# Performance work log

Hardware: AMD Instinct MI355X
Metric: run time of the kernel (lower is better)

The kernel has to match this reference:

```python
import jax, jax.numpy as jnp
import numpy as np

BN_EPS = 1e-5

def conv2d(x, w, pad):
    return jax.lax.conv_general_dilated(x, w, (1, 1), [(pad, pad), (pad, pad)],
                                        dimension_numbers=('NCHW', 'OIHW', 'NCHW'))

def bn(x, g, b, m, v):
    # eval-mode batchnorm with running stats
    c = (None, slice(None), None, None)
    return g[c] * (x - m[c]) * jax.lax.rsqrt(v[c] + BN_EPS) + b[c]

def criss_cross_attention(x, wq, wk, wv, gamma):
    # x: (B, C, H, W); q/k have reduced dim d = C//8
    B, C, H, W = x.shape
    q = jnp.einsum('bchw,dc->bdhw', x, wq)
    k = jnp.einsum('bchw,dc->bdhw', x, wk)
    v = jnp.einsum('bchw,dc->bdhw', x, wv)
    # column (vertical) affinities: for each (h,w), keys at (k,w) -> (B,H,W,H)
    eH = jnp.einsum('bdhw,bdkw->bhwk', q, k)
    # -inf on the h==k diagonal (avoid counting the center pixel twice)
    eH = eH + jnp.where(jnp.eye(H, dtype=bool), -jnp.inf, 0.0)[None, :, None, :]
    # row (horizontal) affinities: keys at (h,k) -> (B,H,W,W)
    eW = jnp.einsum('bdhw,bdhk->bhwk', q, k)
    att = jax.nn.softmax(jnp.concatenate([eH, eW], axis=3), axis=3)  # (B,H,W,H+W)
    aH, aW = att[..., :H], att[..., H:]
    oH = jnp.einsum('bhwk,bdkw->bdhw', aH, v)
    oW = jnp.einsum('bhwk,bdhk->bdhw', aW, v)
    return gamma * (oH + oW) + x

def upsample_bilinear_align_corners(x, out_h, out_w):
    # torch nn.Upsample(mode='bilinear', align_corners=True)
    def interp(x, size, axis):
        n = x.shape[axis]
        pos = jnp.arange(size, dtype=x.dtype) * ((n - 1) / (size - 1))
        lo = jnp.floor(pos).astype(jnp.int32)
        hi = jnp.minimum(lo + 1, n - 1)
        w = pos - lo.astype(x.dtype)
        shp = [1] * x.ndim; shp[axis] = size
        w = w.reshape(shp)
        return jnp.take(x, lo, axis=axis) * (1 - w) + jnp.take(x, hi, axis=axis) * w
    x = interp(x, out_h, 2)
    return interp(x, out_w, 3)

def setup_inputs() -> dict:
    key = jax.random.key(0)
    ks = jax.random.split(key, 16)
    B, C, H, W = 2, 2048, 96, 96
    ic = C // 32          # inter_c = 64
    dq = ic // 8          # 8
    nc = 19
    s = 0.05
    return {
        'x': jax.random.normal(ks[0], (B, C, H, W), jnp.float32),
        'w_in': jax.random.normal(ks[1], (ic, C, 3, 3), jnp.float32) * s,
        'bn_in_g': jnp.ones((ic,), jnp.float32),
        'bn_in_b': jnp.zeros((ic,), jnp.float32),
        'bn_in_m': jax.random.normal(ks[2], (ic,), jnp.float32) * 0.1,
        'bn_in_v': jax.random.uniform(ks[3], (ic,), jnp.float32, 0.5, 1.5),
        'wq': jax.random.normal(ks[4], (dq, ic), jnp.float32) * s,
        'wk': jax.random.normal(ks[5], (dq, ic), jnp.float32) * s,
        'wv': jax.random.normal(ks[6], (ic, ic), jnp.float32) * s,
        'cca_gamma': jax.random.uniform(ks[7], (1,), jnp.float32, 0.2, 0.8),
        'w_out': jax.random.normal(ks[8], (ic, ic, 3, 3), jnp.float32) * s,
        'bn_out_g': jnp.ones((ic,), jnp.float32),
        'bn_out_b': jnp.zeros((ic,), jnp.float32),
        'bn_out_m': jax.random.normal(ks[9], (ic,), jnp.float32) * 0.1,
        'bn_out_v': jax.random.uniform(ks[10], (ic,), jnp.float32, 0.5, 1.5),
        'w_cls1': jax.random.normal(ks[11], (ic, C + ic, 3, 3), jnp.float32) * s,
        'bn_cls_g': jnp.ones((ic,), jnp.float32),
        'bn_cls_b': jnp.zeros((ic,), jnp.float32),
        'bn_cls_m': jax.random.normal(ks[12], (ic,), jnp.float32) * 0.1,
        'bn_cls_v': jax.random.uniform(ks[13], (ic,), jnp.float32, 0.5, 1.5),
        'w_cls2': jax.random.normal(ks[14], (nc, ic, 1, 1), jnp.float32) * s,
    }

def reference(x, w_in, bn_in_g, bn_in_b, bn_in_m, bn_in_v,
              wq, wk, wv, cca_gamma,
              w_out, bn_out_g, bn_out_b, bn_out_m, bn_out_v,
              w_cls1, bn_cls_g, bn_cls_b, bn_cls_m, bn_cls_v, w_cls2):
    RECURRENCE = 2
    out = jax.nn.relu(bn(conv2d(x, w_in, 1), bn_in_g, bn_in_b, bn_in_m, bn_in_v))
    for _ in range(RECURRENCE):
        out = criss_cross_attention(out, wq, wk, wv, cca_gamma)
    out = jax.nn.relu(bn(conv2d(out, w_out, 1), bn_out_g, bn_out_b, bn_out_m, bn_out_v))
    out = jnp.concatenate([x, out], axis=1)
    # cls_seg: conv -> BN (no relu) -> upsample x8 (bilinear, align_corners) -> 1x1 conv
    out = bn(conv2d(out, w_cls1, 1), bn_cls_g, bn_cls_b, bn_cls_m, bn_cls_v)
    H, W = out.shape[2], out.shape[3]
    out = upsample_bilinear_align_corners(out, H * 8, W * 8)
    out = conv2d(out, w_cls2, 0)
    return out
```

## Files before the change

kernel.cpp:

```cpp
#include <hip/hip_runtime.h>
#include <stdint.h>

#define HW 9216

typedef float f32x4 __attribute__((ext_vector_type(4)));
typedef short s16x8 __attribute__((ext_vector_type(8)));

#define PIN() asm volatile("" ::: "memory")
#define WAITV12() asm volatile("s_waitcnt vmcnt(12)" ::: "memory")

__device__ __forceinline__ unsigned short f2bf(float f){
  union { float fv; uint32_t u; } x; x.fv = f;
  uint32_t u = x.u;
  u += 0x7fffu + ((u >> 16) & 1u);
  return (unsigned short)(u >> 16);
}
__device__ __forceinline__ float bf2f(unsigned short s){
  union { uint32_t u; float fv; } x; x.u = ((uint32_t)s) << 16;
  return x.fv;
}

__device__ __forceinline__ void gload16(const void* g, void* l){
  __builtin_amdgcn_global_load_lds(
    (const __attribute__((address_space(1))) unsigned int*)g,
    (__attribute__((address_space(3))) unsigned int*)l, 16, 0, 0);
}

__global__ __launch_bounds__(256) void transp_kernel(const float* __restrict__ x,
    unsigned short* __restrict__ xT){
  __shared__ unsigned short tl[256 * 66];
  int blk = blockIdx.x;
  int b = blk / 1152; int r = blk - b * 1152;
  int cchunk = r / 144, pxt = r - cchunk * 144;
  int c0 = cchunk * 256, px0 = pxt * 64;
  int tid = threadIdx.x;
  for (int e = tid; e < 4096; e += 256){
    int cc = e >> 4, pq = e & 15;
    float4 v4 = *(const float4*)(x + ((size_t)(b * 2048 + c0 + cc)) * HW + px0 + pq * 4);
    const float* vp = (const float*)&v4;
    #pragma unroll
    for (int j = 0; j < 4; j++) tl[cc * 66 + pq * 4 + j] = f2bf(vp[j]);
  }
  __syncthreads();
  for (int j = tid; j < 2048; j += 256){
    int px = j >> 5, oct = j & 31;
    s16x8 pk;
    #pragma unroll
    for (int t = 0; t < 8; t++) pk[t] = (short)tl[(oct * 8 + t) * 66 + px];
    *(s16x8*)(xT + ((size_t)(b * 9216 + px0 + px)) * 2048 + c0 + oct * 8) = pk;
  }
}

__global__ void pack_all_kernel(const float* __restrict__ w_in, const float* __restrict__ w_out,
    const float* __restrict__ w_cls1, unsigned short* __restrict__ WpIn,
    unsigned short* __restrict__ WpOut, unsigned short* __restrict__ WpCls){
  const int N0 = 64 * 2048 * 9, N1 = 64 * 64 * 9, N2 = 64 * 2112 * 9;
  int total = N0 + N1 + N2;
  for (int i = blockIdx.x * blockDim.x + threadIdx.x; i < total; i += gridDim.x * blockDim.x){
    const float* w; unsigned short* Wp; int Cin; int idx;
    if (i < N0){ w = w_in; Wp = WpIn; Cin = 2048; idx = i; }
    else if (i < N0 + N1){ w = w_out; Wp = WpOut; Cin = 64; idx = i - N0; }
    else { w = w_cls1; Wp = WpCls; Cin = 2112; idx = i - N0 - N1; }
    int c = idx & 31; int r = idx >> 5; int o = r & 63; int r2 = r >> 6;
    int tap = r2 % 9; int ck = r2 / 9;
    Wp[idx] = f2bf(w[((size_t)o * Cin + ck * 32 + c) * 9 + tap]);
  }
}

template<int T>
__device__ __forceinline__ void tapbody(const char* hb, s16x8 (&bs)[4], f32x4 (&acc)[4][4],
    const unsigned short* wbase, int gmax, int g0, int wv, int ln, int kg){
  constexpr int dy = T / 3, dx = T - dy * 3;
  #pragma unroll
  for (int mf = 0; mf < 4; mf++){
    int p = (wv * 4 + mf + dy) * 18 + (ln + dx);
    int aoff = p * 64 + ((kg ^ (p & 3)) << 4);
    s16x8 a = *(const s16x8*)(hb + aoff);
    #pragma unroll
    for (int nf = 0; nf < 4; nf++)
      acc[mf][nf] = __builtin_amdgcn_mfma_f32_16x16x32_bf16(a, bs[nf], acc[mf][nf], 0, 0, 0);
  }
  constexpr int dck = (T + 3) / 9, dt = (T + 3) % 9;
  if (g0 + T + 3 < gmax){
    const unsigned short* wb2 = wbase + dck * 18432 + dt * 2048;
    #pragma unroll
    for (int nf = 0; nf < 4; nf++) bs[nf] = *(const s16x8*)(wb2 + nf * 512);
  }
}

__global__ __launch_bounds__(256, 2) void conv_nhwc_kernel(
    const unsigned short* __restrict__ A0, int c0stride,
    const unsigned short* __restrict__ A1, int nck0,
    const unsigned short* __restrict__ Wp,
    unsigned short* __restrict__ sl, int nchunks,
    const unsigned short* __restrict__ zp){
  int mt = blockIdx.x;
  int b = mt / 36; int r = mt - b * 36;
  int h0 = (r / 6) * 16, w0 = (r % 6) * 16;
  int KS = gridDim.y, ks = blockIdx.y;
  int c0 = (nchunks * ks) / KS, c1 = (nchunks * (ks + 1)) / KS;
  int tid = threadIdx.x, lane = tid & 63, wv = tid >> 6;
  int ln = lane & 15, kg = lane >> 4;
  __shared__ char halo[2][24576];

  int pixb0[6], pixb1[6]; bool val[6];
  #pragma unroll
  for (int rr = 0; rr < 6; rr++){
    int i = tid + rr * 256;
    int p = i >> 2, q_lds = i & 3;
    int logq = q_lds ^ (p & 3);
    int hh = p / 18, ww = p - hh * 18;
    int h = h0 - 1 + hh, w = w0 - 1 + ww;
    bool v = (i < 1296) && ((unsigned)h < 96u) && ((unsigned)w < 96u);
    val[rr] = v;
    int pix = (b * 96 + h) * 96 + w;
    pixb0[rr] = v ? (pix * c0stride * 2 + logq * 16) : 0;
    pixb1[rr] = v ? (pix * 128 + logq * 16) : 0;
  }
  const char* a0B = (const char*)A0;
  const char* a1B = (const char*)A1;
  const char* zpB = (const char*)zp;

  auto stage = [&](char* ldsB, int ck){
    bool inA0 = (ck < nck0);
    int chb0 = ck * 64, chb1 = (ck - nck0) * 64;
    #pragma unroll
    for (int rr = 0; rr < 6; rr++){
      const char* src = zpB;
      if (val[rr]) src = inA0 ? (a0B + pixb0[rr] + chb0) : (a1B + pixb1[rr] + chb1);
      gload16(src, ldsB + (tid + rr * 256) * 16);
    }
  };

  f32x4 acc[4][4];
  #pragma unroll
  for (int i = 0; i < 4; i++)
    #pragma unroll
    for (int j = 0; j < 4; j++) acc[i][j] = (f32x4)(0.f);

  s16x8 bs0[4], bs1[4], bs2[4];
  int gmax = (c1 - c0) * 9;

  stage(&halo[0][0], c0);
  PIN();
  {
    const unsigned short* w0b = Wp + (size_t)c0 * 18432 + ln * 32 + kg * 8;
    #pragma unroll
    for (int nf = 0; nf < 4; nf++){
      bs0[nf] = *(const s16x8*)(w0b + 0 * 2048 + nf * 512);
      bs1[nf] = *(const s16x8*)(w0b + 1 * 2048 + nf * 512);
      bs2[nf] = *(const s16x8*)(w0b + 2 * 2048 + nf * 512);
    }
  }
  WAITV12();
  __builtin_amdgcn_s_barrier();

  for (int ck = c0; ck < c1; ck++){
    int cur = (ck - c0) & 1;
    if (ck + 1 < c1){ stage(&halo[cur ^ 1][0], ck + 1); PIN(); }
    const unsigned short* wbase = Wp + (size_t)ck * 18432 + ln * 32 + kg * 8;
    const char* hb = &halo[cur][0];
    int g0 = (ck - c0) * 9;
    tapbody<0>(hb, bs0, acc, wbase, gmax, g0, wv, ln, kg);
    tapbody<1>(hb, bs1, acc, wbase, gmax, g0, wv, ln, kg);
    tapbody<2>(hb, bs2, acc, wbase, gmax, g0, wv, ln, kg);
    tapbody<3>(hb, bs0, acc, wbase, gmax, g0, wv, ln, kg);
    tapbody<4>(hb, bs1, acc, wbase, gmax, g0, wv, ln, kg);
    tapbody<5>(hb, bs2, acc, wbase, gmax, g0, wv, ln, kg);
    tapbody<6>(hb, bs0, acc, wbase, gmax, g0, wv, ln, kg);
    tapbody<7>(hb, bs1, acc, wbase, gmax, g0, wv, ln, kg);
    tapbody<8>(hb, bs2, acc, wbase, gmax, g0, wv, ln, kg);
    if (ck + 1 < c1){
      WAITV12();
      __builtin_amdgcn_s_barrier();
    }
  }

  unsigned short* base = sl + ((size_t)(ks * 72 + mt)) * 16384;
  #pragma unroll
  for (int mf = 0; mf < 4; mf++)
    #pragma unroll
    for (int nf = 0; nf < 4; nf++){
      int o = nf * 16 + ln;
      #pragma unroll
      for (int rr = 0; rr < 4; rr++){
        int m = wv * 64 + mf * 16 + kg * 4 + rr;
        base[m * 64 + o] = f2bf(acc[mf][nf][rr]);
      }
    }
}

__global__ __launch_bounds__(256) void bn_reduce_kernel(const unsigned short* __restrict__ sl,
    int KS, const float* __restrict__ g, const float* __restrict__ bb,
    const float* __restrict__ mm, const float* __restrict__ vv, int relu,
    unsigned short* __restrict__ out, int do_proj,
    const float* __restrict__ wq, const float* __restrict__ wk, const float* __restrict__ wv,
    float* __restrict__ q, float* __restrict__ k, unsigned short* __restrict__ v){
  __shared__ float yl[4 * 65];
  __shared__ float wqL[8 * 65], wkL[8 * 65], wvL[64 * 65];
  int tid = threadIdx.x;
  if (do_proj){
    for (int i = tid; i < 512; i += 256){
      int d = i >> 6, c = i & 63;
      wqL[d * 65 + c] = wq[i]; wkL[d * 65 + c] = wk[i];
    }
    for (int i = tid; i < 4096; i += 256){
      int o = i >> 6, c = i & 63;
      wvL[o * 65 + c] = wv[i];
    }
  }
  int idx = blockIdx.x * 256 + tid;
  int mt = idx >> 14, e = idx & 16383;
  int m = e >> 6, o = e & 63;
  float s = 0.f;
  for (int ks = 0; ks < KS; ks++) s += bf2f(sl[((size_t)(ks * 72 + mt)) * 16384 + e]);
  float sc = g[o] * rsqrtf(vv[o] + 1e-5f);
  float valf = (s - mm[o]) * sc + bb[o];
  if (relu) valf = fmaxf(valf, 0.f);
  int b = mt / 36; int r = mt - b * 36;
  int h = (r / 6) * 16 + (m >> 4), w = (r % 6) * 16 + (m & 15);
  out[(((size_t)b * 96 + h) * 96 + w) * 64 + o] = f2bf(valf);
  if (do_proj){
    int px = tid >> 6;
    yl[px * 65 + o] = valf;
    __syncthreads();
    int m2 = ((blockIdx.x & 63) << 2) + px;
    int h2 = (r / 6) * 16 + (m2 >> 4), w2 = (r % 6) * 16 + (m2 & 15);
    size_t pix2 = ((size_t)b * 96 + h2) * 96 + w2;
    float va = 0.f;
    #pragma unroll 8
    for (int c = 0; c < 64; c++) va += wvL[o * 65 + c] * yl[px * 65 + c];
    v[pix2 * 64 + o] = f2bf(va);
    if (o < 16){
      const float* wsel = (o < 8) ? wqL : wkL;
      int d = o & 7;
      float qa = 0.f;
      #pragma unroll 8
      for (int c = 0; c < 64; c++) qa += wsel[d * 65 + c] * yl[px * 65 + c];
      if (o < 8) q[pix2 * 8 + d] = qa; else k[pix2 * 8 + d] = qa;
    }
  }
}

__global__ __launch_bounds__(256) void bn_reduce_cls_kernel(const unsigned short* __restrict__ sl,
    int KS, const float* __restrict__ g, const float* __restrict__ bb,
    const float* __restrict__ mm, const float* __restrict__ vv,
    const float* __restrict__ w2, float* __restrict__ t19){
  __shared__ float yl[4][64];
  __shared__ float w2L[19 * 64];
  int tid = threadIdx.x;
  for (int i = tid; i < 1216; i += 256) w2L[i] = w2[i];
  int idx = blockIdx.x * 256 + tid;
  int mt = idx >> 14, e = idx & 16383;
  int o = e & 63;
  float s = 0.f;
  for (int ks = 0; ks < KS; ks++) s += bf2f(sl[((size_t)(ks * 72 + mt)) * 16384 + e]);
  float sc = g[o] * rsqrtf(vv[o] + 1e-5f);
  float valf = (s - mm[o]) * sc + bb[o];
  yl[tid >> 6][o] = valf;
  __syncthreads();
  if (tid < 76){
    int mq = tid / 19, j = tid - mq * 19;
    float a = 0.f;
    #pragma unroll 8
    for (int c = 0; c < 64; c++) a += w2L[j * 64 + c] * yl[mq][c];
    int m = ((blockIdx.x & 63) << 2) + mq;
    int b = mt / 36; int r = mt - b * 36;
    int h = (r / 6) * 16 + (m >> 4), w = (r % 6) * 16 + (m & 15);
    t19[((size_t)(b * 19 + j)) * HW + h * 96 + w] = a;
  }
}

__global__ __launch_bounds__(256) void cca_proj_kernel(const unsigned short* __restrict__ xin,
    const float* __restrict__ wq, const float* __restrict__ wk, const float* __restrict__ wv,
    float* __restrict__ q, float* __restrict__ k, unsigned short* __restrict__ v){
  __shared__ float wqL[512], wkL[512], wvL[4096];
  int tid = threadIdx.x;
  for (int i = tid; i < 512; i += 256){ wqL[i] = wq[i]; wkL[i] = wk[i]; }
  for (int i = tid; i < 4096; i += 256) wvL[i] = wv[i];
  __syncthreads();
  int gid = blockIdx.x * 256 + tid;
  int gp = gid >> 1, half = gid & 1;
  unsigned short xv16[64];
  #pragma unroll
  for (int t = 0; t < 8; t++)
    *(s16x8*)(&xv16[t * 8]) = *(const s16x8*)(xin + (size_t)gp * 64 + t * 8);
  float qa[4], ka[4], va[32];
  #pragma unroll
  for (int d = 0; d < 4; d++){ qa[d] = 0.f; ka[d] = 0.f; }
  #pragma unroll
  for (int d = 0; d < 32; d++) va[d] = 0.f;
  int qo = half * 4, vo = half * 32;
  #pragma unroll 4
  for (int c = 0; c < 64; c++){
    float xv = bf2f(xv16[c]);
    #pragma unroll
    for (int d = 0; d < 4; d++){ qa[d] += wqL[(qo + d) * 64 + c] * xv; ka[d] += wkL[(qo + d) * 64 + c] * xv; }
    #pragma unroll
    for (int d = 0; d < 32; d++) va[d] += wvL[(vo + d) * 64 + c] * xv;
  }
  #pragma unroll
  for (int d = 0; d < 4; d++){ q[(size_t)gp * 8 + qo + d] = qa[d]; k[(size_t)gp * 8 + qo + d] = ka[d]; }
  #pragma unroll
  for (int t = 0; t < 4; t++){
    s16x8 pk;
    #pragma unroll
    for (int j = 0; j < 8; j++) pk[j] = (short)f2bf(va[t * 8 + j]);
    *(s16x8*)(v + (size_t)gp * 64 + vo + t * 8) = pk;
  }
}

__global__ __launch_bounds__(256, 2) void cca_colE_kernel(const float* __restrict__ qT,
    const float* __restrict__ kT, float* __restrict__ ebuf){
  int blk = blockIdx.x;
  int b = blk / 192; int r = blk - b * 192; int w = r >> 1, z = r & 1;
  __shared__ float qcL[96 * 12], kcL[48 * 12];
  int tid = threadIdx.x;
  for (int i = tid; i < 768; i += 256){
    int hp = i >> 3, d = i & 7;
    qcL[hp * 12 + d] = qT[((size_t)(b * HW) + hp * 96 + w) * 8 + d];
  }
  for (int i = tid; i < 384; i += 256){
    int j = i >> 3, d = i & 7;
    kcL[j * 12 + d] = kT[((size_t)(b * HW) + (z * 48 + j) * 96 + w) * 8 + d];
  }
  __syncthreads();
  int h0 = (tid & 15) * 6, kl0 = (tid >> 4) * 3;
  f32x4 q0[6], q1[6], k0[3], k1[3];
  #pragma unroll
  for (int i = 0; i < 6; i++){
    q0[i] = *(const f32x4*)&qcL[(h0 + i) * 12];
    q1[i] = *(const f32x4*)&qcL[(h0 + i) * 12 + 4];
  }
  #pragma unroll
  for (int j = 0; j < 3; j++){
    k0[j] = *(const f32x4*)&kcL[(kl0 + j) * 12];
    k1[j] = *(const f32x4*)&kcL[(kl0 + j) * 12 + 4];
  }
  #pragma unroll
  for (int i = 0; i < 6; i++){
    size_t rbase = (((size_t)b * 96 + (h0 + i)) * 96 + w) * 96;
    #pragma unroll
    for (int j = 0; j < 3; j++){
      float e = 0.f;
      #pragma unroll
      for (int d = 0; d < 4; d++) e += q0[i][d] * k0[j][d] + q1[i][d] * k1[j][d];
      int kpg = z * 48 + kl0 + j;
      ebuf[rbase + kpg] = (kpg == h0 + i) ? -1e30f : e;
    }
  }
}

__global__ __launch_bounds__(256, 2) void cca_rowSM_kernel(const float* __restrict__ qT,
    const float* __restrict__ kT, const unsigned short* __restrict__ vT,
    const unsigned short* __restrict__ xin, const float* __restrict__ gamma,
    float* __restrict__ ebuf, unsigned short* __restrict__ xout){
  int blk = blockIdx.x;
  int b = blk / 192; int r = blk - b * 192; int h = r >> 1, z = r & 1;
  __shared__ float qrL[48 * 12], krL[96 * 12];
  __shared__ float ewT[96 * 50];
  __shared__ float vLf[96 * 68];
  __shared__ float aWf[48 * 100];
  int tid = threadIdx.x;
  int lane = tid & 63, wvid = tid >> 6;
  size_t rowb = (size_t)(b * HW) + h * 96;
  const float* ebase = ebuf + rowb * 96;

  float pre0[12], pre1[12];
  #pragma unroll
  for (int t = 0; t < 12; t++){
    int w = z * 48 + wvid + t * 4;
    pre0[t] = ebase[(size_t)w * 96 + lane];
    pre1[t] = (lane < 32) ? ebase[(size_t)w * 96 + 64 + lane] : 0.f;
  }

  for (int i = tid; i < 384; i += 256){
    int wl = i >> 3, d = i & 7;
    qrL[wl * 12 + d] = qT[(rowb + z * 48 + wl) * 8 + d];
  }
  for (int i = tid; i < 768; i += 256){
    int wp = i >> 3, d = i & 7;
    krL[wp * 12 + d] = kT[(rowb + wp) * 8 + d];
  }
  for (int i = tid; i < 768; i += 256){
    int wp = i >> 3, oct = i & 7;
    s16x8 v8 = *(const s16x8*)(vT + (rowb + wp) * 64 + oct * 8);
    #pragma unroll
    for (int j = 0; j < 8; j++) vLf[wp * 68 + oct * 8 + j] = bf2f((unsigned short)v8[j]);
  }
  __syncthreads();
  {
    int wl0 = (tid & 15) * 3, kp0 = (tid >> 4) * 6;
    f32x4 q0[3], q1[3], k0[6], k1[6];
    #pragma unroll
    for (int i = 0; i < 3; i++){
      q0[i] = *(const f32x4*)&qrL[(wl0 + i) * 12];
      q1[i] = *(const f32x4*)&qrL[(wl0 + i) * 12 + 4];
    }
    #pragma unroll
    for (int j = 0; j < 6; j++){
      k0[j] = *(const f32x4*)&krL[(kp0 + j) * 12];
      k1[j] = *(const f32x4*)&krL[(kp0 + j) * 12 + 4];
    }
    #pragma unroll
    for (int j = 0; j < 6; j++)
      #pragma unroll
      for (int i = 0; i < 3; i++){
        float e = 0.f;
        #pragma unroll
        for (int d = 0; d < 4; d++) e += q0[i][d] * k0[j][d] + q1[i][d] * k1[j][d];
        ewT[(kp0 + j) * 50 + (wl0 + i)] = e;
      }
  }
  __syncthreads();
  #pragma unroll
  for (int t = 0; t < 12; t++){
    int wl = wvid + t * 4;
    int w = z * 48 + wl;
    float x0 = pre0[t];
    float x1 = (lane < 32) ? pre1[t] : ewT[(lane - 32) * 50 + wl];
    float x2 = ewT[(lane + 32) * 50 + wl];
    float mx = fmaxf(x0, fmaxf(x1, x2));
    #pragma unroll
    for (int s = 32; s; s >>= 1) mx = fmaxf(mx, __shfl_xor(mx, s));
    float e0 = __expf(x0 - mx), e1 = __expf(x1 - mx), e2 = __expf(x2 - mx);
    float sm = e0 + e1 + e2;
    #pragma unroll
    for (int s = 32; s; s >>= 1) sm += __shfl_xor(sm, s);
    float inv = 1.f / sm;
    float* ebw = (float*)(ebase + (size_t)w * 96);
    ebw[lane] = e0 * inv;
    if (lane < 32) ebw[64 + lane] = e1 * inv;
    else           aWf[wl * 100 + (lane - 32)] = e1 * inv;
    aWf[wl * 100 + (lane + 32)] = e2 * inv;
  }
  __syncthreads();
  float gm = gamma[0];
  int d0 = (tid & 15) * 4, wl0 = (tid >> 4) * 3;
  f32x4 acc2[3];
  #pragma unroll
  for (int c = 0; c < 3; c++) acc2[c] = (f32x4)(0.f);
  for (int kp = 0; kp < 96; kp += 4){
    f32x4 a0 = *(const f32x4*)&aWf[(wl0 + 0) * 100 + kp];
    f32x4 a1 = *(const f32x4*)&aWf[(wl0 + 1) * 100 + kp];
    f32x4 a2 = *(const f32x4*)&aWf[(wl0 + 2) * 100 + kp];
    #pragma unroll
    for (int j = 0; j < 4; j++){
      f32x4 vv = *(const f32x4*)&vLf[(kp + j) * 68 + d0];
      acc2[0] += vv * a0[j];
      acc2[1] += vv * a1[j];
      acc2[2] += vv * a2[j];
    }
  }
  #pragma unroll
  for (int c = 0; c < 3; c++){
    size_t pix = rowb + z * 48 + wl0 + c;
    ushort4 xr = *(const ushort4*)&xin[pix * 64 + d0];
    ushort4 ov;
    ov.x = f2bf(bf2f(xr.x) + gm * acc2[c][0]);
    ov.y = f2bf(bf2f(xr.y) + gm * acc2[c][1]);
    ov.z = f2bf(bf2f(xr.z) + gm * acc2[c][2]);
    ov.w = f2bf(bf2f(xr.w) + gm * acc2[c][3]);
    *(ushort4*)&xout[pix * 64 + d0] = ov;
  }
}

__global__ __launch_bounds__(256, 2) void cca_colO_kernel(const unsigned short* __restrict__ vT,
    const float* __restrict__ gamma, const float* __restrict__ ebuf,
    const unsigned short* __restrict__ xpart, unsigned short* __restrict__ xout){
  int blk = blockIdx.x;
  int b = blk / 192; int r = blk - b * 192; int w = r >> 1, z = r & 1;
  __shared__ float vLf[96 * 68];
  __shared__ float aTf[48 * 100];
  int tid = threadIdx.x;
  for (int i = tid; i < 768; i += 256){
    int kp = i >> 3, oct = i & 7;
    s16x8 v8 = *(const s16x8*)(vT + ((size_t)(b * HW) + kp * 96 + w) * 64 + oct * 8);
    #pragma unroll
    for (int j = 0; j < 8; j++) vLf[kp * 68 + oct * 8 + j] = bf2f((unsigned short)v8[j]);
  }
  for (int i = tid; i < 4608; i += 256){
    int hl = i / 96, kp = i - hl * 96;
    aTf[hl * 100 + kp] = ebuf[(((size_t)b * 96 + z * 48 + hl) * 96 + w) * 96 + kp];
  }
  __syncthreads();
  float gm = gamma[0];
  int d0 = (tid & 15) * 4, hl0 = (tid >> 4) * 3;
  f32x4 acc2[3];
  #pragma unroll
  for (int c = 0; c < 3; c++) acc2[c] = (f32x4)(0.f);
  for (int kp = 0; kp < 96; kp += 4){
    f32x4 a0 = *(const f32x4*)&aTf[(hl0 + 0) * 100 + kp];
    f32x4 a1 = *(const f32x4*)&aTf[(hl0 + 1) * 100 + kp];
    f32x4 a2 = *(const f32x4*)&aTf[(hl0 + 2) * 100 + kp];
    #pragma unroll
    for (int j = 0; j < 4; j++){
      f32x4 vv = *(const f32x4*)&vLf[(kp + j) * 68 + d0];
      acc2[0] += vv * a0[j];
      acc2[1] += vv * a1[j];
      acc2[2] += vv * a2[j];
    }
  }
  #pragma unroll
  for (int c = 0; c < 3; c++){
    size_t pix = (size_t)(b * HW) + (z * 48 + hl0 + c) * 96 + w;
    ushort4 xr = *(const ushort4*)&xpart[pix * 64 + d0];
    ushort4 ov;
    ov.x = f2bf(bf2f(xr.x) + gm * acc2[c][0]);
    ov.y = f2bf(bf2f(xr.y) + gm * acc2[c][1]);
    ov.z = f2bf(bf2f(xr.z) + gm * acc2[c][2]);
    ov.w = f2bf(bf2f(xr.w) + gm * acc2[c][3]);
    *(ushort4*)&xout[pix * 64 + d0] = ov;
  }
}

__global__ void upsample_kernel(const float* __restrict__ t19, float* __restrict__ out){
  int gid = blockIdx.x * 256 + threadIdx.x;
  int xq = gid % 192; int t = gid / 192;
  int yy = t % 768; t /= 768;
  int o = t % 19; int b = t / 19;
  const float R = 95.0f / 767.0f;
  float ry = yy * R;
  int iy = (int)ry;
  float fy = ry - (float)iy;
  int iy1 = min(iy + 1, 95);
  const float* base = t19 + ((size_t)b * 19 + o) * HW;
  float4 res;
  float* rp = (float*)&res;
  #pragma unroll
  for (int j = 0; j < 4; j++){
    int xx = xq * 4 + j;
    float rx = xx * R;
    int ix = (int)rx; float fx = rx - (float)ix; int ix1 = min(ix + 1, 95);
    float v00 = base[iy * 96 + ix],  v01 = base[iy * 96 + ix1];
    float v10 = base[iy1 * 96 + ix], v11 = base[iy1 * 96 + ix1];
    rp[j] = (1.f - fy) * ((1.f - fx) * v00 + fx * v01) + fy * ((1.f - fx) * v10 + fx * v11);
  }
  *(float4*)(out + (((size_t)b * 19 + o) * 768 + yy) * 768 + xq * 4) = res;
}

extern "C" void kernel_launch(void* const* d_in, const int* in_sizes, int n_in,
                              void* d_out, int out_size, void* d_ws, size_t ws_size,
                              hipStream_t stream){
  const float* x       = (const float*)d_in[0];
  const float* w_in    = (const float*)d_in[1];
  const float* bn_in_g = (const float*)d_in[2];
  const float* bn_in_b = (const float*)d_in[3];
  const float* bn_in_m = (const float*)d_in[4];
  const float* bn_in_v = (const float*)d_in[5];
  const float* wq      = (const float*)d_in[6];
  const float* wk      = (const float*)d_in[7];
  const float* wv      = (const float*)d_in[8];
  const float* gamma   = (const float*)d_in[9];
  const float* w_out   = (const float*)d_in[10];
  const float* bn_o_g  = (const float*)d_in[11];
  const float* bn_o_b  = (const float*)d_in[12];
  const float* bn_o_m  = (const float*)d_in[13];
  const float* bn_o_v  = (const float*)d_in[14];
  const float* w_cls1  = (const float*)d_in[15];
  const float* bn_c_g  = (const float*)d_in[16];
  const float* bn_c_b  = (const float*)d_in[17];
  const float* bn_c_m  = (const float*)d_in[18];
  const float* bn_c_v  = (const float*)d_in[19];
  const float* w_cls2  = (const float*)d_in[20];
  float* out = (float*)d_out;

  char* ws = (char*)d_ws;
  size_t off = 0;
  auto alloc = [&](size_t bytes) -> void* {
    void* p = ws + off; off += (bytes + 255) & ~(size_t)255; return p;
  };
  const int KS = 12;
  const size_t NHWCb = (size_t)2 * HW * 64 * 2;
  unsigned short* xT   = (unsigned short*)alloc((size_t)2 * HW * 2048 * 2);
  unsigned short* sl   = (unsigned short*)alloc((size_t)KS * 72 * 16384 * 2);
  float* ebuf = (float*)sl;
  unsigned short* xattA = (unsigned short*)alloc(NHWCb);
  unsigned short* xattB = (unsigned short*)alloc(NHWCb);
  unsigned short* Ptmp  = (unsigned short*)alloc(NHWCb);
  unsigned short* attT  = (unsigned short*)alloc(NHWCb);
  unsigned short* midT  = (unsigned short*)alloc(NHWCb);
  float* qb    = (float*)alloc((size_t)2 * HW * 8 * 4);
  float* kb    = (float*)alloc((size_t)2 * HW * 8 * 4);
  unsigned short* vb = (unsigned short*)alloc(NHWCb);
  float* t19   = (float*)alloc((size_t)2 * 19 * HW * 4);
  unsigned short* WpIn  = (unsigned short*)alloc((size_t)64 * 2048 * 9 * 2);
  unsigned short* WpOut = (unsigned short*)alloc((size_t)64 * 64 * 9 * 2);
  unsigned short* WpCls = (unsigned short*)alloc((size_t)64 * 2112 * 9 * 2);
  unsigned short* zp    = (unsigned short*)alloc(256);
  (void)ws_size; (void)in_sizes; (void)n_in; (void)out_size;

  hipMemsetAsync(zp, 0, 256, stream);
  transp_kernel<<<2304, 256, 0, stream>>>(x, xT);
  pack_all_kernel<<<2048, 256, 0, stream>>>(w_in, w_out, w_cls1, WpIn, WpOut, WpCls);

  conv_nhwc_kernel<<<dim3(72, KS), 256, 0, stream>>>(xT, 2048, nullptr, 64, WpIn, sl, 64, zp);
  bn_reduce_kernel<<<4608, 256, 0, stream>>>(sl, KS, bn_in_g, bn_in_b, bn_in_m, bn_in_v, 1,
      xattA, 1, wq, wk, wv, qb, kb, vb);

  cca_colE_kernel<<<384, 256, 0, stream>>>(qb, kb, ebuf);
  cca_rowSM_kernel<<<384, 256, 0, stream>>>(qb, kb, vb, xattA, gamma, ebuf, Ptmp);
  cca_colO_kernel<<<384, 256, 0, stream>>>(vb, gamma, ebuf, Ptmp, xattB);
  cca_proj_kernel<<<144, 256, 0, stream>>>(xattB, wq, wk, wv, qb, kb, vb);
  cca_colE_kernel<<<384, 256, 0, stream>>>(qb, kb, ebuf);
  cca_rowSM_kernel<<<384, 256, 0, stream>>>(qb, kb, vb, xattB, gamma, ebuf, Ptmp);
  cca_colO_kernel<<<384, 256, 0, stream>>>(vb, gamma, ebuf, Ptmp, attT);

  conv_nhwc_kernel<<<dim3(72, 2), 256, 0, stream>>>(attT, 64, nullptr, 2, WpOut, sl, 2, zp);
  bn_reduce_kernel<<<4608, 256, 0, stream>>>(sl, 2, bn_o_g, bn_o_b, bn_o_m, bn_o_v, 1,
      midT, 0, wq, wk, wv, qb, kb, vb);

  conv_nhwc_kernel<<<dim3(72, KS), 256, 0, stream>>>(xT, 2048, midT, 64, WpCls, sl, 66, zp);
  bn_reduce_cls_kernel<<<4608, 256, 0, stream>>>(sl, KS, bn_c_g, bn_c_b, bn_c_m, bn_c_v, w_cls2, t19);

  upsample_kernel<<<21888, 256, 0, stream>>>(t19, out);
}
```

Measured before the change: 410.1 us.

## Fuse transpose+pack, fuse out-conv with BN/ReLU, shrink halo LDS, retune split-K

Merges the input transpose and weight-packing kernels into one launch. Replaces the split-K output conv plus BN reduce pass with one kernel that applies BN and ReLU in the epilogue and writes NHWC bf16 directly. The halo LDS buffer shrinks to its exact size so occupancy can rise to 3 blocks per CU. Split-K for the large convs drops from 12 to 10. This removes two launches and an intermediate round trip, at the cost of fewer blocks per large conv and possible register pressure.

```diff
diff --git a/kernel.cpp b/kernel.cpp
--- a/kernel.cpp
+++ b/kernel.cpp
@@ -26,44 +26,46 @@
     (__attribute__((address_space(3))) unsigned int*)l, 16, 0, 0);
 }
 
-__global__ __launch_bounds__(256) void transp_kernel(const float* __restrict__ x,
-    unsigned short* __restrict__ xT){
+__global__ __launch_bounds__(256) void transp_pack_kernel(const float* __restrict__ x,
+    unsigned short* __restrict__ xT,
+    const float* __restrict__ w_in, const float* __restrict__ w_out,
+    const float* __restrict__ w_cls1, unsigned short* __restrict__ WpIn,
+    unsigned short* __restrict__ WpOut, unsigned short* __restrict__ WpCls){
   __shared__ unsigned short tl[256 * 66];
   int blk = blockIdx.x;
-  int b = blk / 1152; int r = blk - b * 1152;
-  int cchunk = r / 144, pxt = r - cchunk * 144;
-  int c0 = cchunk * 256, px0 = pxt * 64;
   int tid = threadIdx.x;
-  for (int e = tid; e < 4096; e += 256){
-    int cc = e >> 4, pq = e & 15;
-    float4 v4 = *(const float4*)(x + ((size_t)(b * 2048 + c0 + cc)) * HW + px0 + pq * 4);
-    const float* vp = (const float*)&v4;
-    #pragma unroll
-    for (int j = 0; j < 4; j++) tl[cc * 66 + pq * 4 + j] = f2bf(vp[j]);
-  }
-  __syncthreads();
-  for (int j = tid; j < 2048; j += 256){
-    int px = j >> 5, oct = j & 31;
-    s16x8 pk;
-    #pragma unroll
-    for (int t = 0; t < 8; t++) pk[t] = (short)tl[(oct * 8 + t) * 66 + px];
-    *(s16x8*)(xT + ((size_t)(b * 9216 + px0 + px)) * 2048 + c0 + oct * 8) = pk;
-  }
-}
-
-__global__ void pack_all_kernel(const float* __restrict__ w_in, const float* __restrict__ w_out,
-    const float* __restrict__ w_cls1, unsigned short* __restrict__ WpIn,
-    unsigned short* __restrict__ WpOut, unsigned short* __restrict__ WpCls){
-  const int N0 = 64 * 2048 * 9, N1 = 64 * 64 * 9, N2 = 64 * 2112 * 9;
-  int total = N0 + N1 + N2;
-  for (int i = blockIdx.x * blockDim.x + threadIdx.x; i < total; i += gridDim.x * blockDim.x){
-    const float* w; unsigned short* Wp; int Cin; int idx;
-    if (i < N0){ w = w_in; Wp = WpIn; Cin = 2048; idx = i; }
-    else if (i < N0 + N1){ w = w_out; Wp = WpOut; Cin = 64; idx = i - N0; }
-    else { w = w_cls1; Wp = WpCls; Cin = 2112; idx = i - N0 - N1; }
-    int c = idx & 31; int r = idx >> 5; int o = r & 63; int r2 = r >> 6;
-    int tap = r2 % 9; int ck = r2 / 9;
-    Wp[idx] = f2bf(w[((size_t)o * Cin + ck * 32 + c) * 9 + tap]);
+  if (blk < 2304){
+    int b = blk / 1152; int r = blk - b * 1152;
+    int cchunk = r / 144, pxt = r - cchunk * 144;
+    int c0 = cchunk * 256, px0 = pxt * 64;
+    for (int e = tid; e < 4096; e += 256){
+      int cc = e >> 4, pq = e & 15;
+      float4 v4 = *(const float4*)(x + ((size_t)(b * 2048 + c0 + cc)) * HW + px0 + pq * 4);
+      const float* vp = (const float*)&v4;
+      #pragma unroll
+      for (int j = 0; j < 4; j++) tl[cc * 66 + pq * 4 + j] = f2bf(vp[j]);
+    }
+    __syncthreads();
+    for (int j = tid; j < 2048; j += 256){
+      int px = j >> 5, oct = j & 31;
+      s16x8 pk;
+      #pragma unroll
+      for (int t = 0; t < 8; t++) pk[t] = (short)tl[(oct * 8 + t) * 66 + px];
+      *(s16x8*)(xT + ((size_t)(b * 9216 + px0 + px)) * 2048 + c0 + oct * 8) = pk;
+    }
+  } else {
+    const int N0 = 64 * 2048 * 9, N1 = 64 * 64 * 9, N2 = 64 * 2112 * 9;
+    int total = N0 + N1 + N2;
+    int nblk = gridDim.x - 2304;
+    for (int i = (blk - 2304) * 256 + tid; i < total; i += nblk * 256){
+      const float* w; unsigned short* Wp; int Cin; int idx;
+      if (i < N0){ w = w_in; Wp = WpIn; Cin = 2048; idx = i; }
+      else if (i < N0 + N1){ w = w_out; Wp = WpOut; Cin = 64; idx = i - N0; }
+      else { w = w_cls1; Wp = WpCls; Cin = 2112; idx = i - N0 - N1; }
+      int c = idx & 31; int r = idx >> 5; int o = r & 63; int r2 = r >> 6;
+      int tap = r2 % 9; int ck = r2 / 9;
+      Wp[idx] = f2bf(w[((size_t)o * Cin + ck * 32 + c) * 9 + tap]);
+    }
   }
 }
 
@@ -88,7 +90,7 @@
   }
 }
 
-__global__ __launch_bounds__(256, 2) void conv_nhwc_kernel(
+__global__ __launch_bounds__(256, 3) void conv_nhwc_kernel(
     const unsigned short* __restrict__ A0, int c0stride,
     const unsigned short* __restrict__ A1, int nck0,
     const unsigned short* __restrict__ Wp,
@@ -101,7 +103,7 @@
   int c0 = (nchunks * ks) / KS, c1 = (nchunks * (ks + 1)) / KS;
   int tid = threadIdx.x, lane = tid & 63, wv = tid >> 6;
   int ln = lane & 15, kg = lane >> 4;
-  __shared__ char halo[2][24576];
+  __shared__ char halo[2][20736];
 
   int pixb0[6], pixb1[6]; bool val[6];
   #pragma unroll
@@ -126,9 +128,12 @@
     int chb0 = ck * 64, chb1 = (ck - nck0) * 64;
     #pragma unroll
     for (int rr = 0; rr < 6; rr++){
-      const char* src = zpB;
-      if (val[rr]) src = inA0 ? (a0B + pixb0[rr] + chb0) : (a1B + pixb1[rr] + chb1);
-      gload16(src, ldsB + (tid + rr * 256) * 16);
+      int i = tid + rr * 256;
+      if (i < 1296){
+        const char* src = zpB;
+        if (val[rr]) src = inA0 ? (a0B + pixb0[rr] + chb0) : (a1B + pixb1[rr] + chb1);
+        gload16(src, ldsB + i * 16);
+      }
     }
   };
 
@@ -188,6 +193,109 @@
         base[m * 64 + o] = f2bf(acc[mf][nf][rr]);
       }
     }
+}
+
+__global__ __launch_bounds__(256, 3) void conv_out_kernel(
+    const unsigned short* __restrict__ A0,
+    const unsigned short* __restrict__ Wp,
+    const float* __restrict__ g, const float* __restrict__ bb,
+    const float* __restrict__ mm, const float* __restrict__ vv,
+    unsigned short* __restrict__ outT,
+    const unsigned short* __restrict__ zp){
+  int mt = blockIdx.x;
+  int b = mt / 36; int r = mt - b * 36;
+  int h0 = (r / 6) * 16, w0 = (r % 6) * 16;
+  int tid = threadIdx.x, lane = tid & 63, wv = tid >> 6;
+  int ln = lane & 15, kg = lane >> 4;
+  __shared__ char halo[2][20736];
+
+  int pixb0[6]; bool val[6];
+  #pragma unroll
+  for (int rr = 0; rr < 6; rr++){
+    int i = tid + rr * 256;
+    int p = i >> 2, q_lds = i & 3;
+    int logq = q_lds ^ (p & 3);
+    int hh = p / 18, ww = p - hh * 18;
+    int h = h0 - 1 + hh, w = w0 - 1 + ww;
+    bool v = (i < 1296) && ((unsigned)h < 96u) && ((unsigned)w < 96u);
+    val[rr] = v;
+    int pix = (b * 96 + h) * 96 + w;
+    pixb0[rr] = v ? (pix * 128 + logq * 16) : 0;
+  }
+  const char* a0B = (const char*)A0;
+  const char* zpB = (const char*)zp;
+
+  auto stage = [&](char* ldsB, int ck){
+    int chb0 = ck * 64;
+    #pragma unroll
+    for (int rr = 0; rr < 6; rr++){
+      int i = tid + rr * 256;
+      if (i < 1296){
+        const char* src = val[rr] ? (a0B + pixb0[rr] + chb0) : zpB;
+        gload16(src, ldsB + i * 16);
+      }
+    }
+  };
+
+  f32x4 acc[4][4];
+  #pragma unroll
+  for (int i = 0; i < 4; i++)
+    #pragma unroll
+    for (int j = 0; j < 4; j++) acc[i][j] = (f32x4)(0.f);
+
+  s16x8 bs0[4], bs1[4], bs2[4];
+
+  stage(&halo[0][0], 0);
+  PIN();
+  {
+    const unsigned short* w0b = Wp + ln * 32 + kg * 8;
+    #pragma unroll
+    for (int nf = 0; nf < 4; nf++){
+      bs0[nf] = *(const s16x8*)(w0b + 0 * 2048 + nf * 512);
+      bs1[nf] = *(const s16x8*)(w0b + 1 * 2048 + nf * 512);
+      bs2[nf] = *(const s16x8*)(w0b + 2 * 2048 + nf * 512);
+    }
+  }
+  WAITV12();
+  __builtin_amdgcn_s_barrier();
+
+  for (int ck = 0; ck < 2; ck++){
+    int cur = ck & 1;
+    if (ck == 0){ stage(&halo[1][0], 1); PIN(); }
+    const unsigned short* wbase = Wp + (size_t)ck * 18432 + ln * 32 + kg * 8;
+    const char* hb = &halo[cur][0];
+    int g0 = ck * 9;
+    tapbody<0>(hb, bs0, acc, wbase, 18, g0, wv, ln, kg);
+    tapbody<1>(hb, bs1, acc, wbase, 18, g0, wv, ln, kg);
+    tapbody<2>(hb, bs2, acc, wbase, 18, g0, wv, ln, kg);
+    tapbody<3>(hb, bs0, acc, wbase, 18, g0, wv, ln, kg);
+    tapbody<4>(hb, bs1, acc, wbase, 18, g0, wv, ln, kg);
+    tapbody<5>(hb, bs2, acc, wbase, 18, g0, wv, ln, kg);
+    tapbody<6>(hb, bs0, acc, wbase, 18, g0, wv, ln, kg);
+    tapbody<7>(hb, bs1, acc, wbase, 18, g0, wv, ln, kg);
+    tapbody<8>(hb, bs2, acc, wbase, 18, g0, wv, ln, kg);
+    if (ck == 0){
+      WAITV12();
+      __builtin_amdgcn_s_barrier();
+    }
+  }
+
+  #pragma unroll
+  for (int nf = 0; nf < 4; nf++){
+    int o = nf * 16 + ln;
+    float sc = g[o] * rsqrtf(vv[o] + 1e-5f);
+    float mo = mm[o], bo = bb[o];
+    #pragma unroll
+    for (int mf = 0; mf < 4; mf++)
+      #pragma unroll
+      for (int rr = 0; rr < 4; rr++){
+        int m = wv * 64 + mf * 16 + kg * 4 + rr;
+        int h = h0 + (m >> 4), w = w0 + (m & 15);
+        float valf = (acc[mf][nf][rr] - mo) * sc + bo;
+        valf = fmaxf(valf, 0.f);
+        outT[(((size_t)b * 96 + h) * 96 + w) * 64 + o] = f2bf(valf);
+      }
+  }
 }
 
 __global__ __launch_bounds__(256) void bn_reduce_kernel(const unsigned short* __restrict__ sl,
@@ -570,10 +678,10 @@
   auto alloc = [&](size_t bytes) -> void* {
     void* p = ws + off; off += (bytes + 255) & ~(size_t)255; return p;
   };
-  const int KS = 12;
+  const int KS = 10;
   const size_t NHWCb = (size_t)2 * HW * 64 * 2;
   unsigned short* xT   = (unsigned short*)alloc((size_t)2 * HW * 2048 * 2);
-  unsigned short* sl   = (unsigned short*)alloc((size_t)KS * 72 * 16384 * 2);
+  unsigned short* sl   = (unsigned short*)alloc((size_t)12 * 72 * 16384 * 2);
   float* ebuf = (float*)sl;
   unsigned short* xattA = (unsigned short*)alloc(NHWCb);
   unsigned short* xattB = (unsigned short*)alloc(NHWCb);
@@ -591,8 +699,8 @@
   (void)ws_size; (void)in_sizes; (void)n_in; (void)out_size;
 
   hipMemsetAsync(zp, 0, 256, stream);
-  transp_kernel<<<2304, 256, 0, stream>>>(x, xT);
-  pack_all_kernel<<<2048, 256, 0, stream>>>(w_in, w_out, w_cls1, WpIn, WpOut, WpCls);
+  transp_pack_kernel<<<2304 + 512, 256, 0, stream>>>(x, xT, w_in, w_out, w_cls1,
+      WpIn, WpOut, WpCls);
 
   conv_nhwc_kernel<<<dim3(72, KS), 256, 0, stream>>>(xT, 2048, nullptr, 64, WpIn, sl, 64, zp);
   bn_reduce_kernel<<<4608, 256, 0, stream>>>(sl, KS, bn_in_g, bn_in_b, bn_in_m, bn_in_v, 1,
@@ -606,9 +714,7 @@
   cca_rowSM_kernel<<<384, 256, 0, stream>>>(qb, kb, vb, xattB, gamma, ebuf, Ptmp);
   cca_colO_kernel<<<384, 256, 0, stream>>>(vb, gamma, ebuf, Ptmp, attT);
 
-  conv_nhwc_kernel<<<dim3(72, 2), 256, 0, stream>>>(attT, 64, nullptr, 2, WpOut, sl, 2, zp);
-  bn_reduce_kernel<<<4608, 256, 0, stream>>>(sl, 2, bn_o_g, bn_o_b, bn_o_m, bn_o_v, 1,
-      midT, 0, wq, wk, wv, qb, kb, vb);
+  conv_out_kernel<<<72, 256, 0, stream>>>(attT, WpOut, bn_o_g, bn_o_b, bn_o_m, bn_o_v, midT, zp);
 
   conv_nhwc_kernel<<<dim3(72, KS), 256, 0, stream>>>(xT, 2048, midT, 64, WpCls, sl, 66, zp);
   bn_reduce_cls_kernel<<<4608, 256, 0, stream>>>(sl, KS, bn_c_g, bn_c_b, bn_c_m, bn_c_v, w_cls2, t19);
```

New measurement: 505.3 us. 1.23x slower.
